# Kernel tuning notes

Measured on AMD Instinct MI355X. Metric: run time of the kernel, lower is better.

Reference implementation:

```python
import jax, jax.numpy as jnp
import numpy as np

IN, OUT, H = 512, 128, 128
B = 131072


def setup_inputs() -> dict:
    key = jax.random.key(0)
    ks = jax.random.split(key, 16)
    s = 0.05
    return {
        "x": jax.random.normal(ks[0], (B, IN), dtype=jnp.float32),
        # DNN params
        "fc1_w": jax.random.normal(ks[1], (128, IN), dtype=jnp.float32) * s,
        "fc1_b": jnp.zeros((128,), jnp.float32),
        "fc2_w": jax.random.normal(ks[2], (64, 128), dtype=jnp.float32) * s,
        "fc2_b": jnp.zeros((64,), jnp.float32),
        "fc3_w": jax.random.normal(ks[3], (OUT, 64), dtype=jnp.float32) * s,
        "fc3_b": jnp.zeros((OUT,), jnp.float32),
        # LSTM params (PyTorch gate order: i, f, g, o)
        "W_ih": jax.random.normal(ks[4], (4 * H, IN + OUT), dtype=jnp.float32) * s,
        "W_hh": jax.random.normal(ks[5], (4 * H, H), dtype=jnp.float32) * s,
        "b_ih": jnp.zeros((4 * H,), jnp.float32),
        "b_hh": jnp.zeros((4 * H,), jnp.float32),
        # Attention + final FC
        "attn_w": jax.random.normal(ks[6], (1, H), dtype=jnp.float32) * s,
        "attn_b": jnp.zeros((1,), jnp.float32),
        "fc_w": jax.random.normal(ks[7], (OUT, H), dtype=jnp.float32) * s,
        "fc_b": jnp.zeros((OUT,), jnp.float32),
    }


def reference(x, fc1_w, fc1_b, fc2_w, fc2_b, fc3_w, fc3_b,
              W_ih, W_hh, b_ih, b_hh, attn_w, attn_b, fc_w, fc_b):
    # DNN branch
    d = jax.nn.relu(x @ fc1_w.T + fc1_b)
    d = jax.nn.relu(d @ fc2_w.T + fc2_b)
    d = d @ fc3_w.T + fc3_b                     # [B, OUT]
    xc = jnp.concatenate([x, d], axis=1)        # [B, IN+OUT]
    # Single-step LSTM with h0 = c0 = 0 (W_hh contributes nothing but biases kept)
    gates = xc @ W_ih.T + b_ih + b_hh           # [B, 4H]
    i, f, g, o = jnp.split(gates, 4, axis=1)
    c = jax.nn.sigmoid(i) * jnp.tanh(g)         # f*c0 = 0
    h = jax.nn.sigmoid(o) * jnp.tanh(c)         # [B, H]
    lstm_out = h[:, None, :]                    # [B, 1, H]
    # Attention over seq_len=1 (softmax over a single score == 1)
    scores = jnp.squeeze(lstm_out @ attn_w.T + attn_b, axis=2)  # [B, 1]
    w = jax.nn.softmax(scores, axis=1)
    ctx = jnp.einsum('bs,bsh->bh', w, lstm_out)  # [B, H]
    return ctx @ fc_w.T + fc_b                   # [B, OUT]
```

## Files before the change

### kernel.cpp

```cpp
#include <hip/hip_runtime.h>
#include <hip/hip_bf16.h>

typedef __attribute__((ext_vector_type(8))) short bf16x8;
typedef __attribute__((ext_vector_type(4))) float f32x4;
typedef __attribute__((ext_vector_type(4))) short s16x4;
typedef unsigned short ushort_t;

__device__ __forceinline__ unsigned short f2bf(float f) {
    unsigned int u = __float_as_uint(f);
    u = (u + 0x7FFFu + ((u >> 16) & 1u)) >> 16;
    return (unsigned short)u;
}
__device__ __forceinline__ float fast_sigmoid(float x) {
    return 1.0f / (1.0f + __expf(-x));
}
__device__ __forceinline__ float fast_tanh(float x) {
    x = fminf(fmaxf(x, -15.0f), 15.0f);
    float e = __expf(2.0f * x);
    return (e - 1.0f) / (e + 1.0f);
}
__device__ __forceinline__ f32x4 mfma16(bf16x8 a, bf16x8 b, f32x4 c) {
    return __builtin_amdgcn_mfma_f32_16x16x32_bf16(a, b, c, 0, 0, 0);
}

__global__ void convert_w_kernel(const float* __restrict__ w1, const float* __restrict__ w2,
                                 const float* __restrict__ w3, const float* __restrict__ wih,
                                 const float* __restrict__ fcw, ushort_t* __restrict__ outw) {
    int i = blockIdx.x * 256 + threadIdx.x;
    float v;
    if (i < 65536)       v = w1[i];
    else if (i < 73728)  v = w2[i - 65536];
    else if (i < 81920)  v = w3[i - 73728];
    else if (i < 409600) v = wih[i - 81920];
    else                 v = fcw[i - 409600];
    outw[i] = f2bf(v);
}

#define XS_LD 520
#define D1_LD 136
#define D2_LD 72
#define D3_LD 136
#define HS_LD 136

__global__ __launch_bounds__(512, 4) void fused_mlp_lstm_kernel(
    const float* __restrict__ x,
    const float* __restrict__ b1, const float* __restrict__ b2, const float* __restrict__ b3,
    const float* __restrict__ b_ih, const float* __restrict__ b_hh,
    const float* __restrict__ fc_b,
    const ushort_t* __restrict__ wbf,
    float* __restrict__ out)
{
    __shared__ ushort_t sm[32 * (XS_LD + D1_LD + D2_LD + D3_LD + HS_LD)];
    ushort_t* xs  = sm;
    ushort_t* d1s = xs  + 32 * XS_LD;
    ushort_t* d2s = d1s + 32 * D1_LD;
    ushort_t* d3s = d2s + 32 * D2_LD;
    ushort_t* hs  = d3s + 32 * D3_LD;

    const ushort_t* W1  = wbf;
    const ushort_t* W2  = wbf + 65536;
    const ushort_t* W3  = wbf + 73728;
    const ushort_t* WIH = wbf + 81920;
    const ushort_t* FCW = wbf + 409600;

    const int t  = threadIdx.x;
    const int w  = t >> 6;
    const int l  = t & 63;
    const int q  = l >> 4;
    const int lm = l & 15;
    const int ko = q * 8;
    const int n0 = w * 16;
    const long rowBase = (long)blockIdx.x * 32;

    {
        const float4* xv = (const float4*)(x + rowBase * 512);
        #pragma unroll
        for (int i = 0; i < 8; ++i) {
            int idx = t + i * 512;
            int row = idx >> 7;
            int c4  = idx & 127;
            float4 v = xv[row * 128 + c4];
            s16x4 pk;
            pk.x = (short)f2bf(v.x); pk.y = (short)f2bf(v.y);
            pk.z = (short)f2bf(v.z); pk.w = (short)f2bf(v.w);
            *(s16x4*)(xs + row * XS_LD + c4 * 4) = pk;
        }
    }
    __syncthreads();

    {
        f32x4 a0 = {0,0,0,0}, a1 = {0,0,0,0};
        #pragma unroll
        for (int kk = 0; kk < 16; ++kk) {
            int k0 = kk * 32 + ko;
            bf16x8 fa0 = *(const bf16x8*)(xs + lm * XS_LD + k0);
            bf16x8 fa1 = *(const bf16x8*)(xs + (16 + lm) * XS_LD + k0);
            bf16x8 fb  = *(const bf16x8*)(W1 + (n0 + lm) * 512 + k0);
            a0 = mfma16(fa0, fb, a0);
            a1 = mfma16(fa1, fb, a1);
        }
        float bv = b1[n0 + lm];
        #pragma unroll
        for (int r = 0; r < 4; ++r) {
            d1s[(q * 4 + r) * D1_LD + n0 + lm]      = f2bf(fmaxf(a0[r] + bv, 0.0f));
            d1s[(16 + q * 4 + r) * D1_LD + n0 + lm] = f2bf(fmaxf(a1[r] + bv, 0.0f));
        }
    }
    __syncthreads();

    if (w < 4) {
        f32x4 a0 = {0,0,0,0}, a1 = {0,0,0,0};
        #pragma unroll
        for (int kk = 0; kk < 4; ++kk) {
            int k0 = kk * 32 + ko;
            bf16x8 fa0 = *(const bf16x8*)(d1s + lm * D1_LD + k0);
            bf16x8 fa1 = *(const bf16x8*)(d1s + (16 + lm) * D1_LD + k0);
            bf16x8 fb  = *(const bf16x8*)(W2 + (n0 + lm) * 128 + k0);
            a0 = mfma16(fa0, fb, a0);
            a1 = mfma16(fa1, fb, a1);
        }
        float bv = b2[n0 + lm];
        #pragma unroll
        for (int r = 0; r < 4; ++r) {
            d2s[(q * 4 + r) * D2_LD + n0 + lm]      = f2bf(fmaxf(a0[r] + bv, 0.0f));
            d2s[(16 + q * 4 + r) * D2_LD + n0 + lm] = f2bf(fmaxf(a1[r] + bv, 0.0f));
        }
    }
    __syncthreads();

    {
        f32x4 a0 = {0,0,0,0}, a1 = {0,0,0,0};
        #pragma unroll
        for (int kk = 0; kk < 2; ++kk) {
            int k0 = kk * 32 + ko;
            bf16x8 fa0 = *(const bf16x8*)(d2s + lm * D2_LD + k0);
            bf16x8 fa1 = *(const bf16x8*)(d2s + (16 + lm) * D2_LD + k0);
            bf16x8 fb  = *(const bf16x8*)(W3 + (n0 + lm) * 64 + k0);
            a0 = mfma16(fa0, fb, a0);
            a1 = mfma16(fa1, fb, a1);
        }
        float bv = b3[n0 + lm];
        #pragma unroll
        for (int r = 0; r < 4; ++r) {
            d3s[(q * 4 + r) * D3_LD + n0 + lm]      = f2bf(a0[r] + bv);
            d3s[(16 + q * 4 + r) * D3_LD + n0 + lm] = f2bf(a1[r] + bv);
        }
    }

    f32x4 aI0 = {0,0,0,0}, aI1 = {0,0,0,0};
    f32x4 aG0 = {0,0,0,0}, aG1 = {0,0,0,0};
    f32x4 aO0 = {0,0,0,0}, aO1 = {0,0,0,0};
    const int rI = n0;
    const int rG = 256 + n0;
    const int rO = 384 + n0;
    #pragma unroll
    for (int kk = 0; kk < 16; ++kk) {
        int k0 = kk * 32 + ko;
        bf16x8 fa0 = *(const bf16x8*)(xs + lm * XS_LD + k0);
        bf16x8 fa1 = *(const bf16x8*)(xs + (16 + lm) * XS_LD + k0);
        bf16x8 bi  = *(const bf16x8*)(WIH + (rI + lm) * 640 + k0);
        bf16x8 bg  = *(const bf16x8*)(WIH + (rG + lm) * 640 + k0);
        bf16x8 bo  = *(const bf16x8*)(WIH + (rO + lm) * 640 + k0);
        aI0 = mfma16(fa0, bi, aI0); aI1 = mfma16(fa1, bi, aI1);
        aG0 = mfma16(fa0, bg, aG0); aG1 = mfma16(fa1, bg, aG1);
        aO0 = mfma16(fa0, bo, aO0); aO1 = mfma16(fa1, bo, aO1);
    }
    __syncthreads();
    #pragma unroll
    for (int kk = 0; kk < 4; ++kk) {
        int k0 = kk * 32 + ko;
        bf16x8 fa0 = *(const bf16x8*)(d3s + lm * D3_LD + k0);
        bf16x8 fa1 = *(const bf16x8*)(d3s + (16 + lm) * D3_LD + k0);
        bf16x8 bi  = *(const bf16x8*)(WIH + (rI + lm) * 640 + 512 + k0);
        bf16x8 bg  = *(const bf16x8*)(WIH + (rG + lm) * 640 + 512 + k0);
        bf16x8 bo  = *(const bf16x8*)(WIH + (rO + lm) * 640 + 512 + k0);
        aI0 = mfma16(fa0, bi, aI0); aI1 = mfma16(fa1, bi, aI1);
        aG0 = mfma16(fa0, bg, aG0); aG1 = mfma16(fa1, bg, aG1);
        aO0 = mfma16(fa0, bo, aO0); aO1 = mfma16(fa1, bo, aO1);
    }
    {
        float biasI = b_ih[rI + lm] + b_hh[rI + lm];
        float biasG = b_ih[rG + lm] + b_hh[rG + lm];
        float biasO = b_ih[rO + lm] + b_hh[rO + lm];
        #pragma unroll
        for (int r = 0; r < 4; ++r) {
            float c0 = fast_sigmoid(aI0[r] + biasI) * fast_tanh(aG0[r] + biasG);
            float h0 = fast_sigmoid(aO0[r] + biasO) * fast_tanh(c0);
            float c1 = fast_sigmoid(aI1[r] + biasI) * fast_tanh(aG1[r] + biasG);
            float h1 = fast_sigmoid(aO1[r] + biasO) * fast_tanh(c1);
            hs[(q * 4 + r) * HS_LD + n0 + lm]      = f2bf(h0);
            hs[(16 + q * 4 + r) * HS_LD + n0 + lm] = f2bf(h1);
        }
    }
    __syncthreads();

    {
        f32x4 a0 = {0,0,0,0}, a1 = {0,0,0,0};
        #pragma unroll
        for (int kk = 0; kk < 4; ++kk) {
            int k0 = kk * 32 + ko;
            bf16x8 fa0 = *(const bf16x8*)(hs + lm * HS_LD + k0);
            bf16x8 fa1 = *(const bf16x8*)(hs + (16 + lm) * HS_LD + k0);
            bf16x8 fb  = *(const bf16x8*)(FCW + (n0 + lm) * 128 + k0);
            a0 = mfma16(fa0, fb, a0);
            a1 = mfma16(fa1, fb, a1);
        }
        float bv = fc_b[n0 + lm];
        #pragma unroll
        for (int r = 0; r < 4; ++r) {
            out[(rowBase + q * 4 + r) * 128 + n0 + lm]      = a0[r] + bv;
            out[(rowBase + 16 + q * 4 + r) * 128 + n0 + lm] = a1[r] + bv;
        }
    }
}

extern "C" void kernel_launch(void* const* d_in, const int* in_sizes, int n_in,
                              void* d_out, int out_size, void* d_ws, size_t ws_size,
                              hipStream_t stream) {
    const float* x    = (const float*)d_in[0];
    const float* w1   = (const float*)d_in[1];
    const float* b1   = (const float*)d_in[2];
    const float* w2   = (const float*)d_in[3];
    const float* b2   = (const float*)d_in[4];
    const float* w3   = (const float*)d_in[5];
    const float* b3   = (const float*)d_in[6];
    const float* wih  = (const float*)d_in[7];
    const float* b_ih = (const float*)d_in[9];
    const float* b_hh = (const float*)d_in[10];
    const float* fcw  = (const float*)d_in[13];
    const float* fcb  = (const float*)d_in[14];

    ushort_t* wbf = (ushort_t*)d_ws;
    float* out = (float*)d_out;

    convert_w_kernel<<<1664, 256, 0, stream>>>(w1, w2, w3, wih, fcw, wbf);
    fused_mlp_lstm_kernel<<<131072 / 32, 512, 0, stream>>>(
        x, b1, b2, b3, b_ih, b_hh, fcb, wbf, out);
}
```

Baseline: 681.9 us.

## Double rows per block, register-cache weights, and overlap x load halves

Each block now processes 64 rows instead of 32, so every weight fragment loaded from global memory is reused across four 16-row MFMA tiles instead of two, halving weight traffic per row. Weight fragments are preloaded into registers ahead of barriers. The x tile is loaded in two column halves, with the second half's global loads issued before the first half's GEMM so they overlap. Layer 2 is split across all eight waves. The cost is double the shared memory and much higher register pressure, with launch bounds lowered to 2 blocks per CU, so occupancy drops and spills are possible.

```diff
diff --git a/kernel.cpp b/kernel.cpp
--- a/kernel.cpp
+++ b/kernel.cpp
@@ -42,7 +42,7 @@
 #define D3_LD 136
 #define HS_LD 136
 
-__global__ __launch_bounds__(512, 4) void fused_mlp_lstm_kernel(
+__global__ __launch_bounds__(512, 2) void fused_mlp_lstm_kernel(
     const float* __restrict__ x,
     const float* __restrict__ b1, const float* __restrict__ b2, const float* __restrict__ b3,
     const float* __restrict__ b_ih, const float* __restrict__ b_hh,
@@ -50,12 +50,12 @@
     const ushort_t* __restrict__ wbf,
     float* __restrict__ out)
 {
-    __shared__ ushort_t sm[32 * (XS_LD + D1_LD + D2_LD + D3_LD + HS_LD)];
+    __shared__ ushort_t sm[64 * (XS_LD + D1_LD + D2_LD + D3_LD + HS_LD)];
     ushort_t* xs  = sm;
-    ushort_t* d1s = xs  + 32 * XS_LD;
-    ushort_t* d2s = d1s + 32 * D1_LD;
-    ushort_t* d3s = d2s + 32 * D2_LD;
-    ushort_t* hs  = d3s + 32 * D3_LD;
+    ushort_t* d1s = xs  + 64 * XS_LD;
+    ushort_t* d2s = d1s + 64 * D1_LD;
+    ushort_t* d3s = d2s + 64 * D2_LD;
+    ushort_t* hs  = d3s + 64 * D3_LD;
 
     const ushort_t* W1  = wbf;
     const ushort_t* W2  = wbf + 65536;
@@ -70,147 +70,225 @@
     const int lm = l & 15;
     const int ko = q * 8;
     const int n0 = w * 16;
-    const long rowBase = (long)blockIdx.x * 32;
-
-    {
-        const float4* xv = (const float4*)(x + rowBase * 512);
-        #pragma unroll
-        for (int i = 0; i < 8; ++i) {
-            int idx = t + i * 512;
-            int row = idx >> 7;
-            int c4  = idx & 127;
-            float4 v = xv[row * 128 + c4];
-            s16x4 pk;
-            pk.x = (short)f2bf(v.x); pk.y = (short)f2bf(v.y);
-            pk.z = (short)f2bf(v.z); pk.w = (short)f2bf(v.w);
-            *(s16x4*)(xs + row * XS_LD + c4 * 4) = pk;
-        }
-    }
-    __syncthreads();
-
-    {
-        f32x4 a0 = {0,0,0,0}, a1 = {0,0,0,0};
-        #pragma unroll
-        for (int kk = 0; kk < 16; ++kk) {
-            int k0 = kk * 32 + ko;
-            bf16x8 fa0 = *(const bf16x8*)(xs + lm * XS_LD + k0);
-            bf16x8 fa1 = *(const bf16x8*)(xs + (16 + lm) * XS_LD + k0);
-            bf16x8 fb  = *(const bf16x8*)(W1 + (n0 + lm) * 512 + k0);
-            a0 = mfma16(fa0, fb, a0);
-            a1 = mfma16(fa1, fb, a1);
-        }
+    const long rowBase = (long)blockIdx.x * 64;
+
+    bf16x8 bw1[16];
+    #pragma unroll
+    for (int kk = 0; kk < 16; ++kk)
+        bw1[kk] = *(const bf16x8*)(W1 + (n0 + lm) * 512 + kk * 32 + ko);
+
+    const float4* xv = (const float4*)(x + rowBase * 512);
+    #pragma unroll
+    for (int i = 0; i < 8; ++i) {
+        int u = t + i * 512;
+        int row = u >> 6, c4 = u & 63;
+        float4 v = xv[row * 128 + c4];
+        s16x4 pk;
+        pk.x = (short)f2bf(v.x); pk.y = (short)f2bf(v.y);
+        pk.z = (short)f2bf(v.z); pk.w = (short)f2bf(v.w);
+        *(s16x4*)(xs + row * XS_LD + c4 * 4) = pk;
+    }
+    __syncthreads();
+
+    float4 vb[8];
+    #pragma unroll
+    for (int i = 0; i < 8; ++i) {
+        int u = t + i * 512;
+        vb[i] = xv[(u >> 6) * 128 + 64 + (u & 63)];
+    }
+
+    f32x4 a1[4] = {{0,0,0,0},{0,0,0,0},{0,0,0,0},{0,0,0,0}};
+    #pragma unroll
+    for (int kk = 0; kk < 8; ++kk) {
+        #pragma unroll
+        for (int s = 0; s < 4; ++s) {
+            bf16x8 fa = *(const bf16x8*)(xs + (s * 16 + lm) * XS_LD + kk * 32 + ko);
+            a1[s] = mfma16(fa, bw1[kk], a1[s]);
+        }
+    }
+
+    #pragma unroll
+    for (int i = 0; i < 8; ++i) {
+        int u = t + i * 512;
+        int row = u >> 6, c4 = u & 63;
+        s16x4 pk;
+        pk.x = (short)f2bf(vb[i].x); pk.y = (short)f2bf(vb[i].y);
+        pk.z = (short)f2bf(vb[i].z); pk.w = (short)f2bf(vb[i].w);
+        *(s16x4*)(xs + row * XS_LD + (64 + c4) * 4) = pk;
+    }
+    __syncthreads();
+
+    #pragma unroll
+    for (int kk = 8; kk < 16; ++kk) {
+        #pragma unroll
+        for (int s = 0; s < 4; ++s) {
+            bf16x8 fa = *(const bf16x8*)(xs + (s * 16 + lm) * XS_LD + kk * 32 + ko);
+            a1[s] = mfma16(fa, bw1[kk], a1[s]);
+        }
+    }
+    {
         float bv = b1[n0 + lm];
         #pragma unroll
-        for (int r = 0; r < 4; ++r) {
-            d1s[(q * 4 + r) * D1_LD + n0 + lm]      = f2bf(fmaxf(a0[r] + bv, 0.0f));
-            d1s[(16 + q * 4 + r) * D1_LD + n0 + lm] = f2bf(fmaxf(a1[r] + bv, 0.0f));
-        }
-    }
-    __syncthreads();
-
-    if (w < 4) {
-        f32x4 a0 = {0,0,0,0}, a1 = {0,0,0,0};
+        for (int s = 0; s < 4; ++s)
+            #pragma unroll
+            for (int r = 0; r < 4; ++r)
+                d1s[(s * 16 + q * 4 + r) * D1_LD + n0 + lm] = f2bf(fmaxf(a1[s][r] + bv, 0.0f));
+    }
+
+    const int w4 = w & 3, half = w >> 2;
+    const int n2 = w4 * 16;
+    bf16x8 bw2[4];
+    #pragma unroll
+    for (int kk = 0; kk < 4; ++kk)
+        bw2[kk] = *(const bf16x8*)(W2 + (n2 + lm) * 128 + kk * 32 + ko);
+    __syncthreads();
+
+    {
+        f32x4 a2[2] = {{0,0,0,0},{0,0,0,0}};
         #pragma unroll
         for (int kk = 0; kk < 4; ++kk) {
-            int k0 = kk * 32 + ko;
-            bf16x8 fa0 = *(const bf16x8*)(d1s + lm * D1_LD + k0);
-            bf16x8 fa1 = *(const bf16x8*)(d1s + (16 + lm) * D1_LD + k0);
-            bf16x8 fb  = *(const bf16x8*)(W2 + (n0 + lm) * 128 + k0);
-            a0 = mfma16(fa0, fb, a0);
-            a1 = mfma16(fa1, fb, a1);
-        }
-        float bv = b2[n0 + lm];
-        #pragma unroll
-        for (int r = 0; r < 4; ++r) {
-            d2s[(q * 4 + r) * D2_LD + n0 + lm]      = f2bf(fmaxf(a0[r] + bv, 0.0f));
-            d2s[(16 + q * 4 + r) * D2_LD + n0 + lm] = f2bf(fmaxf(a1[r] + bv, 0.0f));
-        }
-    }
-    __syncthreads();
-
-    {
-        f32x4 a0 = {0,0,0,0}, a1 = {0,0,0,0};
+            #pragma unroll
+            for (int s = 0; s < 2; ++s) {
+                bf16x8 fa = *(const bf16x8*)(d1s + (half * 32 + s * 16 + lm) * D1_LD + kk * 32 + ko);
+                a2[s] = mfma16(fa, bw2[kk], a2[s]);
+            }
+        }
+        float bv = b2[n2 + lm];
+        #pragma unroll
+        for (int s = 0; s < 2; ++s)
+            #pragma unroll
+            for (int r = 0; r < 4; ++r)
+                d2s[(half * 32 + s * 16 + q * 4 + r) * D2_LD + n2 + lm] = f2bf(fmaxf(a2[s][r] + bv, 0.0f));
+    }
+
+    const int rI = n0, rG = 256 + n0, rO = 384 + n0;
+    bf16x8 bw3[2];
+    #pragma unroll
+    for (int kk = 0; kk < 2; ++kk)
+        bw3[kk] = *(const bf16x8*)(W3 + (n0 + lm) * 64 + kk * 32 + ko);
+    bf16x8 bi0[8], bg0[8], bo0[8];
+    #pragma unroll
+    for (int j = 0; j < 8; ++j) {
+        bi0[j] = *(const bf16x8*)(WIH + (rI + lm) * 640 + j * 32 + ko);
+        bg0[j] = *(const bf16x8*)(WIH + (rG + lm) * 640 + j * 32 + ko);
+        bo0[j] = *(const bf16x8*)(WIH + (rO + lm) * 640 + j * 32 + ko);
+    }
+    __syncthreads();
+
+    {
+        f32x4 a3[4] = {{0,0,0,0},{0,0,0,0},{0,0,0,0},{0,0,0,0}};
         #pragma unroll
         for (int kk = 0; kk < 2; ++kk) {
-            int k0 = kk * 32 + ko;
-            bf16x8 fa0 = *(const bf16x8*)(d2s + lm * D2_LD + k0);
-            bf16x8 fa1 = *(const bf16x8*)(d2s + (16 + lm) * D2_LD + k0);
-            bf16x8 fb  = *(const bf16x8*)(W3 + (n0 + lm) * 64 + k0);
-            a0 = mfma16(fa0, fb, a0);
-            a1 = mfma16(fa1, fb, a1);
+            #pragma unroll
+            for (int s = 0; s < 4; ++s) {
+                bf16x8 fa = *(const bf16x8*)(d2s + (s * 16 + lm) * D2_LD + kk * 32 + ko);
+                a3[s] = mfma16(fa, bw3[kk], a3[s]);
+            }
         }
         float bv = b3[n0 + lm];
         #pragma unroll
-        for (int r = 0; r < 4; ++r) {
-            d3s[(q * 4 + r) * D3_LD + n0 + lm]      = f2bf(a0[r] + bv);
-            d3s[(16 + q * 4 + r) * D3_LD + n0 + lm] = f2bf(a1[r] + bv);
-        }
-    }
-
-    f32x4 aI0 = {0,0,0,0}, aI1 = {0,0,0,0};
-    f32x4 aG0 = {0,0,0,0}, aG1 = {0,0,0,0};
-    f32x4 aO0 = {0,0,0,0}, aO1 = {0,0,0,0};
-    const int rI = n0;
-    const int rG = 256 + n0;
-    const int rO = 384 + n0;
-    #pragma unroll
-    for (int kk = 0; kk < 16; ++kk) {
-        int k0 = kk * 32 + ko;
-        bf16x8 fa0 = *(const bf16x8*)(xs + lm * XS_LD + k0);
-        bf16x8 fa1 = *(const bf16x8*)(xs + (16 + lm) * XS_LD + k0);
-        bf16x8 bi  = *(const bf16x8*)(WIH + (rI + lm) * 640 + k0);
-        bf16x8 bg  = *(const bf16x8*)(WIH + (rG + lm) * 640 + k0);
-        bf16x8 bo  = *(const bf16x8*)(WIH + (rO + lm) * 640 + k0);
-        aI0 = mfma16(fa0, bi, aI0); aI1 = mfma16(fa1, bi, aI1);
-        aG0 = mfma16(fa0, bg, aG0); aG1 = mfma16(fa1, bg, aG1);
-        aO0 = mfma16(fa0, bo, aO0); aO1 = mfma16(fa1, bo, aO1);
-    }
-    __syncthreads();
-    #pragma unroll
-    for (int kk = 0; kk < 4; ++kk) {
-        int k0 = kk * 32 + ko;
-        bf16x8 fa0 = *(const bf16x8*)(d3s + lm * D3_LD + k0);
-        bf16x8 fa1 = *(const bf16x8*)(d3s + (16 + lm) * D3_LD + k0);
-        bf16x8 bi  = *(const bf16x8*)(WIH + (rI + lm) * 640 + 512 + k0);
-        bf16x8 bg  = *(const bf16x8*)(WIH + (rG + lm) * 640 + 512 + k0);
-        bf16x8 bo  = *(const bf16x8*)(WIH + (rO + lm) * 640 + 512 + k0);
-        aI0 = mfma16(fa0, bi, aI0); aI1 = mfma16(fa1, bi, aI1);
-        aG0 = mfma16(fa0, bg, aG0); aG1 = mfma16(fa1, bg, aG1);
-        aO0 = mfma16(fa0, bo, aO0); aO1 = mfma16(fa1, bo, aO1);
+        for (int s = 0; s < 4; ++s)
+            #pragma unroll
+            for (int r = 0; r < 4; ++r)
+                d3s[(s * 16 + q * 4 + r) * D3_LD + n0 + lm] = f2bf(a3[s][r] + bv);
+    }
+
+    f32x4 aI[4] = {{0,0,0,0},{0,0,0,0},{0,0,0,0},{0,0,0,0}};
+    f32x4 aG[4] = {{0,0,0,0},{0,0,0,0},{0,0,0,0},{0,0,0,0}};
+    f32x4 aO[4] = {{0,0,0,0},{0,0,0,0},{0,0,0,0},{0,0,0,0}};
+    #pragma unroll
+    for (int j = 0; j < 8; ++j) {
+        bf16x8 fa[4];
+        #pragma unroll
+        for (int s = 0; s < 4; ++s)
+            fa[s] = *(const bf16x8*)(xs + (s * 16 + lm) * XS_LD + j * 32 + ko);
+        #pragma unroll
+        for (int s = 0; s < 4; ++s) {
+            aI[s] = mfma16(fa[s], bi0[j], aI[s]);
+            aG[s] = mfma16(fa[s], bg0[j], aG[s]);
+            aO[s] = mfma16(fa[s], bo0[j], aO[s]);
+        }
+    }
+    {
+        bf16x8 bi1[8], bg1[8], bo1[8];
+        #pragma unroll
+        for (int j = 0; j < 8; ++j) {
+            bi1[j] = *(const bf16x8*)(WIH + (rI + lm) * 640 + (8 + j) * 32 + ko);
+            bg1[j] = *(const bf16x8*)(WIH + (rG + lm) * 640 + (8 + j) * 32 + ko);
+            bo1[j] = *(const bf16x8*)(WIH + (rO + lm) * 640 + (8 + j) * 32 + ko);
+        }
+        #pragma unroll
+        for (int j = 0; j < 8; ++j) {
+            bf16x8 fa[4];
+            #pragma unroll
+            for (int s = 0; s < 4; ++s)
+                fa[s] = *(const bf16x8*)(xs + (s * 16 + lm) * XS_LD + (8 + j) * 32 + ko);
+            #pragma unroll
+            for (int s = 0; s < 4; ++s) {
+                aI[s] = mfma16(fa[s], bi1[j], aI[s]);
+                aG[s] = mfma16(fa[s], bg1[j], aG[s]);
+                aO[s] = mfma16(fa[s], bo1[j], aO[s]);
+            }
+        }
+    }
+    {
+        bf16x8 biB[4], bgB[4], boB[4];
+        #pragma unroll
+        for (int j = 0; j < 4; ++j) {
+            biB[j] = *(const bf16x8*)(WIH + (rI + lm) * 640 + 512 + j * 32 + ko);
+            bgB[j] = *(const bf16x8*)(WIH + (rG + lm) * 640 + 512 + j * 32 + ko);
+            boB[j] = *(const bf16x8*)(WIH + (rO + lm) * 640 + 512 + j * 32 + ko);
+        }
+        __syncthreads();
+        #pragma unroll
+        for (int j = 0; j < 4; ++j) {
+            bf16x8 fa[4];
+            #pragma unroll
+            for (int s = 0; s < 4; ++s)
+                fa[s] = *(const bf16x8*)(d3s + (s * 16 + lm) * D3_LD + j * 32 + ko);
+            #pragma unroll
+            for (int s = 0; s < 4; ++s) {
+                aI[s] = mfma16(fa[s], biB[j], aI[s]);
+                aG[s] = mfma16(fa[s], bgB[j], aG[s]);
+                aO[s] = mfma16(fa[s], boB[j], aO[s]);
+            }
+        }
     }
     {
         float biasI = b_ih[rI + lm] + b_hh[rI + lm];
         float biasG = b_ih[rG + lm] + b_hh[rG + lm];
         float biasO = b_ih[rO + lm] + b_hh[rO + lm];
         #pragma unroll
-        for (int r = 0; r < 4; ++r) {
-            float c0 = fast_sigmoid(aI0[r] + biasI) * fast_tanh(aG0[r] + biasG);
-            float h0 = fast_sigmoid(aO0[r] + biasO) * fast_tanh(c0);
-            float c1 = fast_sigmoid(aI1[r] + biasI) * fast_tanh(aG1[r] + biasG);
-            float h1 = fast_sigmoid(aO1[r] + biasO) * fast_tanh(c1);
-            hs[(q * 4 + r) * HS_LD + n0 + lm]      = f2bf(h0);
-            hs[(16 + q * 4 + r) * HS_LD + n0 + lm] = f2bf(h1);
-        }
-    }
-    __syncthreads();
-
-    {
-        f32x4 a0 = {0,0,0,0}, a1 = {0,0,0,0};
+        for (int s = 0; s < 4; ++s)
+            #pragma unroll
+            for (int r = 0; r < 4; ++r) {
+                float c = fast_sigmoid(aI[s][r] + biasI) * fast_tanh(aG[s][r] + biasG);
+                float h = fast_sigmoid(aO[s][r] + biasO) * fast_tanh(c);
+                hs[(s * 16 + q * 4 + r) * HS_LD + n0 + lm] = f2bf(h);
+            }
+    }
+    bf16x8 bw5[4];
+    #pragma unroll
+    for (int kk = 0; kk < 4; ++kk)
+        bw5[kk] = *(const bf16x8*)(FCW + (n0 + lm) * 128 + kk * 32 + ko);
+    __syncthreads();
+
+    {
+        f32x4 a5[4] = {{0,0,0,0},{0,0,0,0},{0,0,0,0},{0,0,0,0}};
         #pragma unroll
         for (int kk = 0; kk < 4; ++kk) {
-            int k0 = kk * 32 + ko;
-            bf16x8 fa0 = *(const bf16x8*)(hs + lm * HS_LD + k0);
-            bf16x8 fa1 = *(const bf16x8*)(hs + (16 + lm) * HS_LD + k0);
-            bf16x8 fb  = *(const bf16x8*)(FCW + (n0 + lm) * 128 + k0);
-            a0 = mfma16(fa0, fb, a0);
-            a1 = mfma16(fa1, fb, a1);
+            #pragma unroll
+            for (int s = 0; s < 4; ++s) {
+                bf16x8 fa = *(const bf16x8*)(hs + (s * 16 + lm) * HS_LD + kk * 32 + ko);
+                a5[s] = mfma16(fa, bw5[kk], a5[s]);
+            }
         }
         float bv = fc_b[n0 + lm];
         #pragma unroll
-        for (int r = 0; r < 4; ++r) {
-            out[(rowBase + q * 4 + r) * 128 + n0 + lm]      = a0[r] + bv;
-            out[(rowBase + 16 + q * 4 + r) * 128 + n0 + lm] = a1[r] + bv;
-        }
+        for (int s = 0; s < 4; ++s)
+            #pragma unroll
+            for (int r = 0; r < 4; ++r)
+                out[(rowBase + s * 16 + q * 4 + r) * 128 + n0 + lm] = a5[s][r] + bv;
     }
 }
 
@@ -234,6 +312,6 @@
     float* out = (float*)d_out;
 
     convert_w_kernel<<<1664, 256, 0, stream>>>(w1, w2, w3, wih, fcw, wbf);
-    fused_mlp_lstm_kernel<<<131072 / 32, 512, 0, stream>>>(
+    fused_mlp_lstm_kernel<<<131072 / 64, 512, 0, stream>>>(
         x, b1, b2, b3, b_ih, b_hh, fcb, wbf, out);
 }
```

After: 577.3 us. -15.3%, faster.
